# Kernel optimization log

Hardware: AMD Instinct MI355X
Metric: run time of the kernel (lower is better)

Reference implementation:

```python
import jax, jax.numpy as jnp
import numpy as np

N_HEAD = 32
N_KV = 8
HEAD_DIM = 64  # n_embd // n_head = 2048 // 32
EPS = 1e-6


def bit_linear(x, w):
    """BitNet b1.58 BitLinear (no bias): int8 absmax activation quant (per-token),
    ternary mean-absmax weight quant, straight-through estimator."""
    s = 127.0 / jnp.clip(jnp.max(jnp.abs(x), axis=-1, keepdims=True), 1e-5)
    xq = jnp.clip(jnp.round(x * s), -128.0, 127.0) / s
    xq = x + jax.lax.stop_gradient(xq - x)
    ws = 1.0 / jnp.clip(jnp.mean(jnp.abs(w)), 1e-5)
    wq = jnp.clip(jnp.round(w * ws), -1.0, 1.0) / ws
    wq = w + jax.lax.stop_gradient(wq - w)
    return xq @ wq.T


def sub_ln(x, gamma, beta):
    mean = jnp.mean(x, axis=-1, keepdims=True)
    var = jnp.mean((x - mean) ** 2, axis=-1, keepdims=True)
    return (x - mean) / jnp.sqrt(var + EPS) * gamma + beta


def setup_inputs() -> dict:
    key = jax.random.key(0)
    ks = jax.random.split(key, 8)
    D, KV, F = 2048, 512, 8192
    B, T = 1, 2048
    w_scale = 0.02
    return {
        "x": jax.random.normal(ks[0], (B, T, D), jnp.float32),
        "g1": jnp.ones((D,), jnp.float32),
        "b1": jnp.zeros((D,), jnp.float32),
        "g2": jnp.ones((D,), jnp.float32),
        "b2": jnp.zeros((D,), jnp.float32),
        "wq": jax.random.normal(ks[1], (D, D), jnp.float32) * w_scale,
        "wk": jax.random.normal(ks[2], (KV, D), jnp.float32) * w_scale,
        "wv": jax.random.normal(ks[3], (KV, D), jnp.float32) * w_scale,
        "wo": jax.random.normal(ks[4], (D, D), jnp.float32) * w_scale,
        "w1": jax.random.normal(ks[5], (F, D), jnp.float32) * w_scale,
        "w2": jax.random.normal(ks[6], (D, F), jnp.float32) * w_scale,
    }


def reference(x, g1, b1, g2, b2, wq, wk, wv, wo, w1, w2):
    B, T, D = x.shape
    # --- attention sublayer (pre-norm, residual) ---
    h = sub_ln(x, g1, b1)
    q = bit_linear(h, wq).reshape(B, T, N_HEAD, HEAD_DIM)
    k = bit_linear(h, wk).reshape(B, T, N_KV, HEAD_DIM)
    v = bit_linear(h, wv).reshape(B, T, N_KV, HEAD_DIM)
    rep = N_HEAD // N_KV
    k = jnp.repeat(k, rep, axis=2)  # GQA repeat_interleave
    v = jnp.repeat(v, rep, axis=2)
    attn = jnp.einsum('bqhd,bkhd->bhqk', q, k) * (HEAD_DIM ** -0.5)
    causal = jnp.tril(jnp.ones((T, T), bool))
    attn = jnp.where(causal, attn, -jnp.inf)
    attn = jax.nn.softmax(attn, axis=-1)
    o = jnp.einsum('bhqk,bkhd->bqhd', attn, v).reshape(B, T, D)
    x = x + bit_linear(o, wo)
    # --- FFN sublayer (pre-norm, residual, ReLU^2) ---
    h2 = sub_ln(x, g2, b2)
    f = bit_linear(h2, w1)
    f = jnp.maximum(f, 0.0) ** 2
    return x + bit_linear(f, w2)
```

## Files before the change

kernel.cpp:

```cpp
#include <hip/hip_runtime.h>
#include <hip/hip_bf16.h>
#include <stdint.h>

typedef __bf16 bf16;
typedef signed char i8;
typedef __bf16 v8bf __attribute__((ext_vector_type(8)));
typedef __bf16 v4bf __attribute__((ext_vector_type(4)));
typedef signed char v8i8 __attribute__((ext_vector_type(8)));
typedef int    v4i  __attribute__((ext_vector_type(4)));
typedef float  f32x16 __attribute__((ext_vector_type(16)));

#define MFMA32(a,b,c)   __builtin_amdgcn_mfma_f32_32x32x16_bf16((a),(b),(c),0,0,0)
#define MFMA_I8(a,b,c)  __builtin_amdgcn_mfma_i32_16x16x64_i8((a),(b),(c),0,0,0)

#define INV_D2 (1.0f / 4194304.0f)
#define INV_KV (1.0f / 1048576.0f)
#define INV_F  (1.0f / 16777216.0f)

__device__ __forceinline__ void glds16(const void* g, void* l) {
  __builtin_amdgcn_global_load_lds(
      (const __attribute__((address_space(1))) void*)g,
      (__attribute__((address_space(3))) void*)l, 16, 0, 0);
}

__device__ __forceinline__ float wred_sum(float v) {
#pragma unroll
  for (int o = 32; o; o >>= 1) v += __shfl_xor(v, o);
  return v;
}
__device__ __forceinline__ float wred_max(float v) {
#pragma unroll
  for (int o = 32; o; o >>= 1) v = fmaxf(v, __shfl_xor(v, o));
  return v;
}

__device__ __forceinline__ unsigned int packbf(float a, float b) {
  union { bf16 h[2]; unsigned int u; } x;
  x.h[0] = (bf16)a; x.h[1] = (bf16)b;
  return x.u;
}

__global__ void k_sniff(const unsigned short* __restrict__ x, int* __restrict__ flag) {
  int cnt = 0;
  for (int i = threadIdx.x; i < 2048; i += 64) {
    const unsigned short u = x[i];
    const int e = (u >> 7) & 0xFF;
    if (u == 0 || (e >= 100 && e <= 140)) cnt++;
  }
#pragma unroll
  for (int o = 32; o; o >>= 1) cnt += __shfl_xor(cnt, o);
  if (threadIdx.x == 0) flag[0] = (cnt >= 1844) ? 0 : 1;
}


__global__ void k_zero(float* p, int n) {
  int i = threadIdx.x;
  if (i < n) p[i] = 0.0f;
}

__global__ __launch_bounds__(256) void k_zerof(float4* __restrict__ p) {
  p[(size_t)blockIdx.x * 256 + threadIdx.x] = make_float4(0.f, 0.f, 0.f, 0.f);
}

__global__ __launch_bounds__(256) void k_abssum6(const void* __restrict__ p0, const void* __restrict__ p1,
                                                 const void* __restrict__ p2, const void* __restrict__ p3,
                                                 const void* __restrict__ p4, const void* __restrict__ p5,
                                                 const int* __restrict__ flag, float* __restrict__ out) {
  const int b = blockIdx.x, tid = threadIdx.x;
  const void* w; int seg, base;
  if (b < 64)       { w = p0; seg = 0; base = b; }
  else if (b < 80)  { w = p1; seg = 1; base = b - 64; }
  else if (b < 96)  { w = p2; seg = 2; base = b - 80; }
  else if (b < 160) { w = p3; seg = 3; base = b - 96; }
  else if (b < 416) { w = p4; seg = 4; base = b - 160; }
  else              { w = p5; seg = 5; base = b - 416; }
  const int f32 = flag[0];
  __shared__ float sred[4];
  float s = 0.0f;
  if (f32) {
    const float4* p = (const float4*)w + (size_t)base * 16384;
#pragma unroll 4
    for (int i = 0; i < 64; i++) {
      float4 a = p[i * 256 + tid];
      s += fabsf(a.x) + fabsf(a.y) + fabsf(a.z) + fabsf(a.w);
    }
  } else {
    const v8bf* p = (const v8bf*)w + (size_t)base * 8192;
#pragma unroll 4
    for (int i = 0; i < 32; i++) {
      v8bf v = p[i * 256 + tid];
#pragma unroll
      for (int j = 0; j < 8; j++) s += fabsf((float)v[j]);
    }
  }
  s = wred_sum(s);
  if ((tid & 63) == 0) sred[tid >> 6] = s;
  __syncthreads();
  if (tid == 0) atomicAdd(out + seg, sred[0] + sred[1] + sred[2] + sred[3]);
}

__global__ __launch_bounds__(256) void k_wquant6(const void* __restrict__ p0, const void* __restrict__ p1,
                                                 const void* __restrict__ p2, const void* __restrict__ p3,
                                                 const void* __restrict__ p4, const void* __restrict__ p5,
                                                 i8* __restrict__ d0, i8* __restrict__ d1,
                                                 i8* __restrict__ d2, i8* __restrict__ d3,
                                                 i8* __restrict__ d4, i8* __restrict__ d5,
                                                 const float* __restrict__ wsum,
                                                 const int* __restrict__ flag) {
  const int b = blockIdx.x;
  const void* w; i8* o; int seg, base; float invn;
  if (b < 2048)       { w = p0; o = d0; seg = 0; base = b;         invn = INV_D2; }
  else if (b < 2560)  { w = p1; o = d1; seg = 1; base = b - 2048;  invn = INV_KV; }
  else if (b < 3072)  { w = p2; o = d2; seg = 2; base = b - 2560;  invn = INV_KV; }
  else if (b < 5120)  { w = p3; o = d3; seg = 3; base = b - 3072;  invn = INV_D2; }
  else if (b < 13312) { w = p4; o = d4; seg = 4; base = b - 5120;  invn = INV_F; }
  else                { w = p5; o = d5; seg = 5; base = b - 13312; invn = INV_F; }
  const int gid = base * 256 + threadIdx.x;
  const int i = gid * 8;
  const float ws = 1.0f / fmaxf(wsum[seg] * invn, 1e-5f);
  const int f32 = flag[0];
  float v[8];
  if (f32) {
    float4 a = ((const float4*)w)[gid * 2];
    float4 b4 = ((const float4*)w)[gid * 2 + 1];
    v[0] = a.x; v[1] = a.y; v[2] = a.z; v[3] = a.w;
    v[4] = b4.x; v[5] = b4.y; v[6] = b4.z; v[7] = b4.w;
  } else {
    v8bf t = *(const v8bf*)((const bf16*)w + i);
#pragma unroll
    for (int j = 0; j < 8; j++) v[j] = (float)t[j];
  }
  v8i8 r;
#pragma unroll
  for (int j = 0; j < 8; j++) {
    float t = rintf(v[j] * ws);
    r[j] = (i8)fminf(fmaxf(t, -1.0f), 1.0f);
  }
  *(v8i8*)(o + i) = r;
}

template <bool XINT>
__global__ __launch_bounds__(256) void k_lnq(const void* __restrict__ x, const void* __restrict__ g,
                                             const void* __restrict__ b, i8* __restrict__ q,
                                             float* __restrict__ sc, const int* __restrict__ flag) {
  const int row = blockIdx.x, tid = threadIdx.x;
  const int f32 = flag[0];
  __shared__ float sred[4];
  float v[8];
#pragma unroll
  for (int i = 0; i < 8; i++) {
    const size_t idx = (size_t)row * 2048 + tid + 256 * i;
    if (XINT)      v[i] = ((const float*)x)[idx];
    else if (f32)  v[i] = ((const float*)x)[idx];
    else           v[i] = (float)((const bf16*)x)[idx];
  }
  float s = 0.0f;
#pragma unroll
  for (int i = 0; i < 8; i++) s += v[i];
  s = wred_sum(s);
  if ((tid & 63) == 0) sred[tid >> 6] = s;
  __syncthreads();
  const float mean = (sred[0] + sred[1] + sred[2] + sred[3]) * (1.0f / 2048.0f);
  __syncthreads();
  float vs = 0.0f;
#pragma unroll
  for (int i = 0; i < 8; i++) { float d = v[i] - mean; vs += d * d; }
  vs = wred_sum(vs);
  if ((tid & 63) == 0) sred[tid >> 6] = vs;
  __syncthreads();
  const float rstd = rsqrtf((sred[0] + sred[1] + sred[2] + sred[3]) * (1.0f / 2048.0f) + 1e-6f);
  __syncthreads();
  float hq[8];
  float am = 0.0f;
#pragma unroll
  for (int i = 0; i < 8; i++) {
    const int c = tid + 256 * i;
    const float gv = f32 ? ((const float*)g)[c] : (float)((const bf16*)g)[c];
    const float bv = f32 ? ((const float*)b)[c] : (float)((const bf16*)b)[c];
    hq[i] = (v[i] - mean) * rstd * gv + bv;
    am = fmaxf(am, fabsf(hq[i]));
  }
  am = wred_max(am);
  if ((tid & 63) == 0) sred[tid >> 6] = am;
  __syncthreads();
  am = fmaxf(fmaxf(sred[0], sred[1]), fmaxf(sred[2], sred[3]));
  const float cl = fmaxf(am, 1e-5f);
  const float s127 = 127.0f / cl;
#pragma unroll
  for (int i = 0; i < 8; i++) {
    float r = rintf(hq[i] * s127);
    r = fminf(fmaxf(r, -128.0f), 127.0f);
    q[(size_t)row * 2048 + tid + 256 * i] = (i8)r;
  }
  if (tid == 0) sc[row] = cl * (1.0f / 127.0f);
}

template <int IT>
__global__ __launch_bounds__(256) void k_rowq(const bf16* __restrict__ in, i8* __restrict__ q,
                                              float* __restrict__ sc) {
  const int row = blockIdx.x, tid = threadIdx.x;
  const int C = IT * 256;
  __shared__ float sred[4];
  const bf16* xr = in + (size_t)row * C;
  float v[IT];
  float am = 0.0f;
#pragma unroll
  for (int i = 0; i < IT; i++) {
    v[i] = (float)xr[tid + 256 * i];
    am = fmaxf(am, fabsf(v[i]));
  }
  am = wred_max(am);
  if ((tid & 63) == 0) sred[tid >> 6] = am;
  __syncthreads();
  am = fmaxf(fmaxf(sred[0], sred[1]), fmaxf(sred[2], sred[3]));
  const float cl = fmaxf(am, 1e-5f);
  const float s127 = 127.0f / cl;
#pragma unroll
  for (int i = 0; i < IT; i++) {
    float r = rintf(v[i] * s127);
    r = fminf(fmaxf(r, -128.0f), 127.0f);
    q[(size_t)row * C + tid + 256 * i] = (i8)r;
  }
  if (tid == 0) sc[row] = cl * (1.0f / 127.0f);
}

template <int EPI>
__global__ __launch_bounds__(256) void k_gemm(const i8* __restrict__ A, const i8* __restrict__ B,
                                              const float* __restrict__ sA,
                                              const float* __restrict__ wsum, float winv,
                                              void* __restrict__ out,
                                              int M, int N, int K, int Kc,
                                              const int* __restrict__ flag) {
  __shared__ __align__(16) i8 As[2][128 * 64];
  __shared__ __align__(16) i8 Bs[2][128 * 64];
  const int tid = threadIdx.x;
  const int lane = tid & 63;
  const int ml = lane & 15;
  const int q4 = lane >> 4;
  const int wid = tid >> 6;
  const int wM = wid >> 1;
  const int wN = wid & 1;
  const int m0 = blockIdx.y * 128;
  const int n0 = blockIdx.x * 128;

  const int r0 = tid >> 2;
  const int c0 = (tid & 3) * 16;
  const i8* Ag0 = A + (size_t)(m0 + r0) * K + c0;
  const i8* Ag1 = Ag0 + (size_t)64 * K;
  const i8* Bg0 = B + (size_t)(n0 + r0) * K + c0;
  const i8* Bg1 = Bg0 + (size_t)64 * K;
  const int l0 = wid * 1024;
  const int l1 = 4096 + wid * 1024;

  v4i acc[4][4] = {};

  const int kbeg = blockIdx.z * Kc;
  const int kfin = kbeg + Kc;
  glds16(Ag0 + kbeg, &As[0][l0]);
  glds16(Ag1 + kbeg, &As[0][l1]);
  glds16(Bg0 + kbeg, &Bs[0][l0]);
  glds16(Bg1 + kbeg, &Bs[0][l1]);
  __syncthreads();
  int cb = 0;
  for (int k0 = kbeg; k0 < kfin; k0 += 64) {
    const int kn = k0 + 64;
    if (kn < kfin) {
      glds16(Ag0 + kn, &As[cb ^ 1][l0]);
      glds16(Ag1 + kn, &As[cb ^ 1][l1]);
      glds16(Bg0 + kn, &Bs[cb ^ 1][l0]);
      glds16(Bg1 + kn, &Bs[cb ^ 1][l1]);
    }
    v4i af[4], bfr[4];
#pragma unroll
    for (int i = 0; i < 4; i++) af[i] = *(const v4i*)&As[cb][(wM * 64 + i * 16 + ml) * 64 + q4 * 16];
#pragma unroll
    for (int j = 0; j < 4; j++) bfr[j] = *(const v4i*)&Bs[cb][(wN * 64 + j * 16 + ml) * 64 + q4 * 16];
#pragma unroll
    for (int i = 0; i < 4; i++)
#pragma unroll
      for (int j = 0; j < 4; j++) acc[i][j] = MFMA_I8(af[i], bfr[j], acc[i][j]);
    __syncthreads();
    cb ^= 1;
  }

  if (EPI == 4) {
    int* ob = (int*)out;
#pragma unroll
    for (int i = 0; i < 4; i++)
#pragma unroll
      for (int r = 0; r < 4; r++) {
        const int row = m0 + wM * 64 + i * 16 + q4 * 4 + r;
#pragma unroll
        for (int j = 0; j < 4; j++) {
          const int col = n0 + wN * 64 + j * 16 + ml;
          atomicAdd(ob + (size_t)row * N + col, acc[i][j][r]);
        }
      }
    return;
  }

  const float cw = fmaxf(wsum[0] * winv, 1e-5f);
#pragma unroll
  for (int i = 0; i < 4; i++) {
#pragma unroll
    for (int r = 0; r < 4; r++) {
      const int row = m0 + wM * 64 + i * 16 + q4 * 4 + r;
      const float sa = sA[row] * cw;
#pragma unroll
      for (int j = 0; j < 4; j++) {
        const int col = n0 + wN * 64 + j * 16 + ml;
        const float val = (float)acc[i][j][r] * sa;
        float u = fmaxf(val, 0.0f);
        ((bf16*)out)[(size_t)row * N + col] = (bf16)(u * u);
      }
    }
  }
}

template <int MODE>
__global__ __launch_bounds__(256) void k_epi(const int* __restrict__ acc, int lda, int cofs,
                                             int ncols,
                                             const float* __restrict__ sA,
                                             const float* __restrict__ wsum, float winv,
                                             const void* __restrict__ resid,
                                             void* __restrict__ out,
                                             const int* __restrict__ flag) {
  const int row = blockIdx.x, tid = threadIdx.x;
  const float cw = fmaxf(wsum[0] * winv, 1e-5f);
  const float srow = sA[row] * cw;
  const int f32 = flag[0];
  for (int c = tid * 4; c < ncols; c += 1024) {
    const v4i a = *(const v4i*)(acc + (size_t)row * lda + cofs + c);
    const float v0 = (float)a[0] * srow, v1 = (float)a[1] * srow;
    const float v2 = (float)a[2] * srow, v3 = (float)a[3] * srow;
    const size_t o = (size_t)row * ncols + c;
    if (MODE == 1) {
      float4 rv;
      if (f32) {
        rv = *(const float4*)((const float*)resid + o);
      } else {
        const v4bf rb = *(const v4bf*)((const bf16*)resid + o);
        rv = make_float4((float)rb[0], (float)rb[1], (float)rb[2], (float)rb[3]);
      }
      *(float4*)((float*)out + o) = make_float4(rv.x + v0, rv.y + v1, rv.z + v2, rv.w + v3);
    } else {
      const float4 rv = *(const float4*)((const float*)resid + o);
      const float o0 = rv.x + v0, o1 = rv.y + v1, o2 = rv.z + v2, o3 = rv.w + v3;
      if (f32) {
        *(float4*)((float*)out + o) = make_float4(o0, o1, o2, o3);
      } else {
        v4bf r;
        r[0] = (bf16)o0; r[1] = (bf16)o1; r[2] = (bf16)o2; r[3] = (bf16)o3;
        *(v4bf*)((bf16*)out + o) = r;
      }
    }
  }
}

__global__ __launch_bounds__(256) void k_epiQK(const int* __restrict__ acc,
                                               const float* __restrict__ sA,
                                               const float* __restrict__ wsum,
                                               bf16* __restrict__ Qb, bf16* __restrict__ Kh) {
  const int row = blockIdx.x, tid = threadIdx.x;
  const float cw0 = fmaxf(wsum[0] * INV_D2, 1e-5f);
  const float cw1 = fmaxf(wsum[1] * INV_KV, 1e-5f);
  const float sa = sA[row];
  bf16* kb_ = Kh + ((size_t)(row >> 5) * 2048) + (row & 31) * 64;
  const int rx = row & 7;
  for (int c = tid * 4; c < 2560; c += 1024) {
    const v4i a = *(const v4i*)(acc + (size_t)row * 2560 + c);
    if (c < 2048) {
      v4bf r;
#pragma unroll
      for (int j = 0; j < 4; j++) r[j] = (bf16)((float)a[j] * sa * cw0);
      *(v4bf*)(Qb + (size_t)row * 2048 + c) = r;
    } else {
      const int j0 = c - 2048;
      const int kvh = j0 >> 6, d = j0 & 63;
      v4bf r;
#pragma unroll
      for (int j = 0; j < 4; j++) r[j] = (bf16)((float)a[j] * sa * cw1);
      const int elem = ((((d >> 3) ^ rx) << 3) + (d & 7));
      *(v4bf*)(kb_ + (size_t)kvh * 131072 + elem) = r;
    }
  }
}

__global__ __launch_bounds__(256) void k_epiVt(const int* __restrict__ acc,
                                               const float* __restrict__ sT,
                                               const float* __restrict__ wsum,
                                               bf16* __restrict__ Vtb) {
  const int vr = blockIdx.x, tid = threadIdx.x;
  const int kvh = vr >> 6, dd = vr & 63;
  const float cw = fmaxf(wsum[2] * INV_KV, 1e-5f);
  const int sw = (dd >> 1) & 3;
  bf16* vb = Vtb + (size_t)kvh * 131072 + dd * 32;
  for (int c = tid * 4; c < 2048; c += 1024) {
    const v4i a = *(const v4i*)(acc + (size_t)vr * 2048 + c);
    const float4 sc = *(const float4*)(sT + c);
    v4bf r;
    r[0] = (bf16)((float)a[0] * sc.x * cw);
    r[1] = (bf16)((float)a[1] * sc.y * cw);
    r[2] = (bf16)((float)a[2] * sc.z * cw);
    r[3] = (bf16)((float)a[3] * sc.w * cw);
    const int tq = c & 31;
    const int elem = (c >> 5) * 2048 + ((((tq >> 3) ^ sw) << 3) + (tq & 7));
    *(v4bf*)(vb + elem) = r;
  }
}

__global__ __launch_bounds__(64) void k_attn(const bf16* __restrict__ Q, const bf16* __restrict__ Kh,
                                             const bf16* __restrict__ Vtb, bf16* __restrict__ O) {
  __shared__ __align__(16) bf16 Kl[2][2048];
  __shared__ __align__(16) bf16 Vl[2][2048];
  const int h = blockIdx.y;
  const int kvh = h >> 2;
  const int t = (blockIdx.x + ((h >> 2) << 3)) & 63;
  const int qw0 = t * 32;
  const int lane = threadIdx.x;
  const int ql = lane & 31;
  const int hi = lane >> 5;

  v8bf qf[4];
  {
    const bf16* qp = Q + (size_t)(qw0 + ql) * 2048 + h * 64 + hi * 8;
#pragma unroll
    for (int c = 0; c < 4; c++) qf[c] = *(const v8bf*)(qp + c * 16);
  }

  float m = -1e30f, l = 0.0f;
  f32x16 acc0 = {}, acc1 = {};

  const bf16* khead = Kh + (size_t)kvh * 131072 + lane * 8;
  const bf16* vhead = Vtb + (size_t)kvh * 131072 + lane * 8;

#pragma unroll
  for (int cc = 0; cc < 4; cc++) {
    glds16(khead + cc * 512, &Kl[0][cc * 512]);
    glds16(vhead + cc * 512, &Vl[0][cc * 512]);
  }
  asm volatile("s_waitcnt vmcnt(0)" ::: "memory");
  int cb = 0;

  for (int kb = 0; kb <= qw0; kb += 32) {
    if (kb + 32 <= qw0) {
      const int tb = ((kb + 32) >> 5) * 2048;
#pragma unroll
      for (int cc = 0; cc < 4; cc++) {
        glds16(khead + tb + cc * 512, &Kl[cb ^ 1][cc * 512]);
        glds16(vhead + tb + cc * 512, &Vl[cb ^ 1][cc * 512]);
      }
    }
    f32x16 s = {};
    {
      const char* kl = (const char*)&Kl[cb][0] + ql * 128;
#pragma unroll
      for (int c = 0; c < 4; c++) {
        const int sl = ((2 * c + hi) ^ (ql & 7)) << 4;
        const v8bf kf = *(const v8bf*)(kl + sl);
        s = MFMA32(kf, qf[c], s);
      }
    }
    const bool diag = (kb == qw0);
    float p[16];
    float rm = -1e30f;
#pragma unroll
    for (int r = 0; r < 16; r++) {
      float v = s[r] * 0.125f;
      const int koff = (r & 3) + ((r >> 2) << 3) + (hi << 2);
      if (diag && koff > ql) v = -1e30f;
      p[r] = v;
      rm = fmaxf(rm, v);
    }
    rm = fmaxf(rm, __shfl_xor(rm, 32));
    const float mn = fmaxf(m, rm);
    const float alpha = __expf(m - mn);
    m = mn;
    float rs = 0.0f;
#pragma unroll
    for (int r = 0; r < 16; r++) {
      p[r] = __expf(p[r] - mn);
      rs += p[r];
    }
    rs += __shfl_xor(rs, 32);
    l = l * alpha + rs;
#pragma unroll
    for (int r = 0; r < 16; r++) { acc0[r] *= alpha; acc1[r] *= alpha; }

    unsigned int w0 = packbf(p[0], p[1]),   w2 = packbf(p[4], p[5]);
    unsigned int w1 = packbf(p[2], p[3]),   w3 = packbf(p[6], p[7]);
    unsigned int x0 = packbf(p[8], p[9]),   x2 = packbf(p[12], p[13]);
    unsigned int x1 = packbf(p[10], p[11]), x3 = packbf(p[14], p[15]);
    asm("v_permlane32_swap_b32 %0, %1" : "+v"(w0), "+v"(w2));
    asm("v_permlane32_swap_b32 %0, %1" : "+v"(w1), "+v"(w3));
    asm("v_permlane32_swap_b32 %0, %1" : "+v"(x0), "+v"(x2));
    asm("v_permlane32_swap_b32 %0, %1" : "+v"(x1), "+v"(x3));
    union BU { unsigned int u[4]; v8bf v; } B0, B1;
    B0.u[0] = w0; B0.u[1] = w1; B0.u[2] = w2; B0.u[3] = w3;
    B1.u[0] = x0; B1.u[1] = x1; B1.u[2] = x2; B1.u[3] = x3;

    {
      const char* vl = (const char*)&Vl[cb][0] + ql * 64;
      const int sx = (ql >> 1) & 3;
      const int sl0 = ((0 + hi) ^ sx) << 4;
      const int sl1 = ((2 + hi) ^ sx) << 4;
      const v8bf v00 = *(const v8bf*)(vl + sl0);
      const v8bf v01 = *(const v8bf*)(vl + sl1);
      const v8bf v10 = *(const v8bf*)(vl + 2048 + sl0);
      const v8bf v11 = *(const v8bf*)(vl + 2048 + sl1);
      acc0 = MFMA32(v00, B0.v, acc0);
      acc0 = MFMA32(v01, B1.v, acc0);
      acc1 = MFMA32(v10, B0.v, acc1);
      acc1 = MFMA32(v11, B1.v, acc1);
    }
    asm volatile("s_waitcnt vmcnt(0)" ::: "memory");
    cb ^= 1;
  }

  const float inv = 1.0f / l;
  unsigned int* op = (unsigned int*)(O + (size_t)(qw0 + ql) * 2048 + h * 64);
#pragma unroll
  for (int r = 0; r < 16; r += 2) {
    const int d = (r & 3) + ((r >> 2) << 3) + (hi << 2);
    op[d >> 1] = packbf(acc0[r] * inv, acc0[r + 1] * inv);
    op[(d >> 1) + 16] = packbf(acc1[r] * inv, acc1[r + 1] * inv);
  }
}

extern "C" void kernel_launch(void* const* d_in, const int* in_sizes, int n_in, void* d_out,
                              int out_size, void* d_ws, size_t ws_size, hipStream_t stream) {
  const void* x = d_in[0];
  const void* g1 = d_in[1];
  const void* b1 = d_in[2];
  const void* g2 = d_in[3];
  const void* b2 = d_in[4];
  const void* wq = d_in[5];
  const void* wk = d_in[6];
  const void* wv = d_in[7];
  const void* wo = d_in[8];
  const void* w1 = d_in[9];
  const void* w2 = d_in[10];

  char* ws = (char*)d_ws;
  const size_t MB = 1ull << 20;
  float* wsum = (float*)ws;
  float* s1 = (float*)(ws + 8192);
  float* so = (float*)(ws + 16384);
  float* s2 = (float*)(ws + 24576);
  float* sf = (float*)(ws + 32768);
  int* flag = (int*)(ws + 40960);
  char* big = ws + 65536;

  i8* w1z = (i8*)(big);
  i8* fq  = (i8*)(big);
  i8* w2z = (i8*)(big + 16 * MB);
  i8* wqz = (i8*)(big + 32 * MB);
  i8* wkz = (i8*)(big + 36 * MB);
  i8* wvz = (i8*)(big + 37 * MB);
  i8* woz = (i8*)(big + 38 * MB);
  i8* xq1 = (i8*)(big + 42 * MB);
  i8* oq  = xq1;
  int* accQK = (int*)(big + 46 * MB);
  int* accVt = (int*)(big + 66 * MB);
  bf16* Kh   = (bf16*)(big + 70 * MB);
  bf16* Vtb  = (bf16*)(big + 72 * MB);
  bf16* Qb   = (bf16*)(big + 74 * MB);
  bf16* Ob   = (bf16*)(big + 82 * MB);
  int* accO  = (int*)(big + 46 * MB);
  float* x1  = (float*)(big + 80 * MB);
  i8* xq2 = (i8*)(big + 74 * MB);
  bf16* Fb   = (bf16*)(big + 42 * MB);
  int* accF  = (int*)(big + 42 * MB);

  k_sniff<<<1, 64, 0, stream>>>((const unsigned short*)x, flag);
  k_zero<<<1, 64, 0, stream>>>(wsum, 8);
  k_zerof<<<6144, 256, 0, stream>>>((float4*)accQK);

  k_abssum6<<<672, 256, 0, stream>>>(wq, wk, wv, wo, w1, w2, flag, wsum);
  k_wquant6<<<21504, 256, 0, stream>>>(wq, wk, wv, wo, w1, w2,
                                       wqz, wkz, wvz, woz, w1z, w2z, wsum, flag);

  k_lnq<false><<<2048, 256, 0, stream>>>(x, g1, b1, xq1, s1, flag);
  k_gemm<4><<<dim3(20, 16, 4), 256, 0, stream>>>(xq1, wqz, s1, wsum + 0, INV_D2, accQK,
                                                 2048, 2560, 2048, 512, flag);
  k_gemm<4><<<dim3(16, 4, 4), 256, 0, stream>>>(wvz, xq1, s1, wsum + 2, INV_KV, accVt,
                                                512, 2048, 2048, 512, flag);
  k_epiQK<<<2048, 256, 0, stream>>>(accQK, s1, wsum, Qb, Kh);
  k_epiVt<<<512, 256, 0, stream>>>(accVt, s1, wsum, Vtb);
  k_attn<<<dim3(64, 32), 64, 0, stream>>>(Qb, Kh, Vtb, Ob);
  k_rowq<8><<<2048, 256, 0, stream>>>(Ob, oq, so);
  k_zerof<<<4096, 256, 0, stream>>>((float4*)accO);
  k_gemm<4><<<dim3(16, 16, 4), 256, 0, stream>>>(oq, woz, so, wsum + 3, INV_D2, accO,
                                                 2048, 2048, 2048, 512, flag);
  k_epi<1><<<2048, 256, 0, stream>>>(accO, 2048, 0, 2048, so, wsum + 3, INV_D2, x, x1, flag);

  k_lnq<true><<<2048, 256, 0, stream>>>(x1, g2, b2, xq2, s2, flag);
  k_gemm<2><<<dim3(64, 16, 1), 256, 0, stream>>>(xq2, w1z, s2, wsum + 4, INV_F, Fb,
                                                 2048, 8192, 2048, 2048, flag);
  k_rowq<32><<<2048, 256, 0, stream>>>(Fb, fq, sf);
  k_zerof<<<4096, 256, 0, stream>>>((float4*)accF);
  k_gemm<4><<<dim3(16, 16, 4), 256, 0, stream>>>(fq, w2z, sf, wsum + 5, INV_F, accF,
                                                 2048, 2048, 8192, 2048, flag);
  k_epi<2><<<2048, 256, 0, stream>>>(accF, 2048, 0, 2048, sf, wsum + 5, INV_F, x1, d_out, flag);
}
```

Measured before the change: 657.1 us.

## Deepen int8 GEMM prefetch with explicit vmcnt waits and fuse residual epilogue into LayerNorm quant

The int8 GEMM main loop now issues the next LDS tile load after the barrier, two stages ahead of use. It waits on vmcnt counts instead of a full __syncthreads, so global-to-LDS loads can overlap the MFMA work. Separately, the out-projection residual epilogue is fused with the second sub-LN and int8 row quantization into one kernel, which drops a launch and a reread of x1. The manual waitcnt and barrier scheduling is fragile: the buffer reuse with two buffers and a two-ahead issue depends on the barrier placement being correct.

```diff
diff --git a/kernel.cpp b/kernel.cpp
--- a/kernel.cpp
+++ b/kernel.cpp
@@ -252,24 +252,32 @@
   const int l0 = wid * 1024;
   const int l1 = 4096 + wid * 1024;
 
+  const int kbeg = blockIdx.z * Kc;
+  const int nst = Kc >> 6;
+
+  auto issue = [&](int tt) {
+    const int k0 = kbeg + (tt << 6);
+    const int bb = tt & 1;
+    glds16(Ag0 + k0, &As[bb][l0]);
+    glds16(Ag1 + k0, &As[bb][l1]);
+    glds16(Bg0 + k0, &Bs[bb][l0]);
+    glds16(Bg1 + k0, &Bs[bb][l1]);
+  };
+
+  issue(0);
+  if (nst > 1) {
+    issue(1);
+    asm volatile("s_waitcnt vmcnt(4)" ::: "memory");
+  } else {
+    asm volatile("s_waitcnt vmcnt(0)" ::: "memory");
+  }
+  __builtin_amdgcn_s_barrier();
+  __builtin_amdgcn_sched_barrier(0);
+
   v4i acc[4][4] = {};
 
-  const int kbeg = blockIdx.z * Kc;
-  const int kfin = kbeg + Kc;
-  glds16(Ag0 + kbeg, &As[0][l0]);
-  glds16(Ag1 + kbeg, &As[0][l1]);
-  glds16(Bg0 + kbeg, &Bs[0][l0]);
-  glds16(Bg1 + kbeg, &Bs[0][l1]);
-  __syncthreads();
-  int cb = 0;
-  for (int k0 = kbeg; k0 < kfin; k0 += 64) {
-    const int kn = k0 + 64;
-    if (kn < kfin) {
-      glds16(Ag0 + kn, &As[cb ^ 1][l0]);
-      glds16(Ag1 + kn, &As[cb ^ 1][l1]);
-      glds16(Bg0 + kn, &Bs[cb ^ 1][l0]);
-      glds16(Bg1 + kn, &Bs[cb ^ 1][l1]);
-    }
+  for (int t = 0; t < nst; ++t) {
+    const int cb = t & 1;
     v4i af[4], bfr[4];
 #pragma unroll
     for (int i = 0; i < 4; i++) af[i] = *(const v4i*)&As[cb][(wM * 64 + i * 16 + ml) * 64 + q4 * 16];
@@ -279,8 +287,19 @@
     for (int i = 0; i < 4; i++)
 #pragma unroll
       for (int j = 0; j < 4; j++) acc[i][j] = MFMA_I8(af[i], bfr[j], acc[i][j]);
-    __syncthreads();
-    cb ^= 1;
+    __builtin_amdgcn_sched_barrier(0);
+    __builtin_amdgcn_s_barrier();
+    __builtin_amdgcn_sched_barrier(0);
+    if (t + 2 < nst) {
+      issue(t + 2);
+      asm volatile("s_waitcnt vmcnt(4)" ::: "memory");
+      __builtin_amdgcn_s_barrier();
+      __builtin_amdgcn_sched_barrier(0);
+    } else if (t + 1 < nst) {
+      asm volatile("s_waitcnt vmcnt(0)" ::: "memory");
+      __builtin_amdgcn_s_barrier();
+      __builtin_amdgcn_sched_barrier(0);
+    }
   }
 
   if (EPI == 4) {
@@ -334,27 +353,78 @@
     const float v0 = (float)a[0] * srow, v1 = (float)a[1] * srow;
     const float v2 = (float)a[2] * srow, v3 = (float)a[3] * srow;
     const size_t o = (size_t)row * ncols + c;
-    if (MODE == 1) {
-      float4 rv;
-      if (f32) {
-        rv = *(const float4*)((const float*)resid + o);
-      } else {
-        const v4bf rb = *(const v4bf*)((const bf16*)resid + o);
-        rv = make_float4((float)rb[0], (float)rb[1], (float)rb[2], (float)rb[3]);
-      }
-      *(float4*)((float*)out + o) = make_float4(rv.x + v0, rv.y + v1, rv.z + v2, rv.w + v3);
+    const float4 rv = *(const float4*)((const float*)resid + o);
+    const float o0 = rv.x + v0, o1 = rv.y + v1, o2 = rv.z + v2, o3 = rv.w + v3;
+    if (f32) {
+      *(float4*)((float*)out + o) = make_float4(o0, o1, o2, o3);
     } else {
-      const float4 rv = *(const float4*)((const float*)resid + o);
-      const float o0 = rv.x + v0, o1 = rv.y + v1, o2 = rv.z + v2, o3 = rv.w + v3;
-      if (f32) {
-        *(float4*)((float*)out + o) = make_float4(o0, o1, o2, o3);
-      } else {
-        v4bf r;
-        r[0] = (bf16)o0; r[1] = (bf16)o1; r[2] = (bf16)o2; r[3] = (bf16)o3;
-        *(v4bf*)((bf16*)out + o) = r;
-      }
-    }
-  }
+      v4bf r;
+      r[0] = (bf16)o0; r[1] = (bf16)o1; r[2] = (bf16)o2; r[3] = (bf16)o3;
+      *(v4bf*)((bf16*)out + o) = r;
+    }
+  }
+}
+
+__global__ __launch_bounds__(256) void k_epi1ln(const int* __restrict__ acc,
+                                                const float* __restrict__ so_,
+                                                const float* __restrict__ wsum,
+                                                const void* __restrict__ xres,
+                                                float* __restrict__ x1,
+                                                const void* __restrict__ g, const void* __restrict__ b,
+                                                i8* __restrict__ q, float* __restrict__ sc,
+                                                const int* __restrict__ flag) {
+  const int row = blockIdx.x, tid = threadIdx.x;
+  const int f32 = flag[0];
+  __shared__ float sred[4];
+  const float srow = so_[row] * fmaxf(wsum[3] * INV_D2, 1e-5f);
+  float v[8];
+#pragma unroll
+  for (int i = 0; i < 8; i++) {
+    const size_t idx = (size_t)row * 2048 + tid + 256 * i;
+    const float a = (float)acc[idx] * srow;
+    const float rv = f32 ? ((const float*)xres)[idx] : (float)((const bf16*)xres)[idx];
+    v[i] = rv + a;
+    x1[idx] = v[i];
+  }
+  float s = 0.0f;
+#pragma unroll
+  for (int i = 0; i < 8; i++) s += v[i];
+  s = wred_sum(s);
+  if ((tid & 63) == 0) sred[tid >> 6] = s;
+  __syncthreads();
+  const float mean = (sred[0] + sred[1] + sred[2] + sred[3]) * (1.0f / 2048.0f);
+  __syncthreads();
+  float vs = 0.0f;
+#pragma unroll
+  for (int i = 0; i < 8; i++) { float d = v[i] - mean; vs += d * d; }
+  vs = wred_sum(vs);
+  if ((tid & 63) == 0) sred[tid >> 6] = vs;
+  __syncthreads();
+  const float rstd = rsqrtf((sred[0] + sred[1] + sred[2] + sred[3]) * (1.0f / 2048.0f) + 1e-6f);
+  __syncthreads();
+  float hq[8];
+  float am = 0.0f;
+#pragma unroll
+  for (int i = 0; i < 8; i++) {
+    const int c = tid + 256 * i;
+    const float gv = f32 ? ((const float*)g)[c] : (float)((const bf16*)g)[c];
+    const float bv = f32 ? ((const float*)b)[c] : (float)((const bf16*)b)[c];
+    hq[i] = (v[i] - mean) * rstd * gv + bv;
+    am = fmaxf(am, fabsf(hq[i]));
+  }
+  am = wred_max(am);
+  if ((tid & 63) == 0) sred[tid >> 6] = am;
+  __syncthreads();
+  am = fmaxf(fmaxf(sred[0], sred[1]), fmaxf(sred[2], sred[3]));
+  const float cl = fmaxf(am, 1e-5f);
+  const float s127 = 127.0f / cl;
+#pragma unroll
+  for (int i = 0; i < 8; i++) {
+    float r = rintf(hq[i] * s127);
+    r = fminf(fmaxf(r, -128.0f), 127.0f);
+    q[(size_t)row * 2048 + tid + 256 * i] = (i8)r;
+  }
+  if (tid == 0) sc[row] = cl * (1.0f / 127.0f);
 }
 
 __global__ __launch_bounds__(256) void k_epiQK(const int* __restrict__ acc,
@@ -592,9 +662,8 @@
   k_zerof<<<4096, 256, 0, stream>>>((float4*)accO);
   k_gemm<4><<<dim3(16, 16, 4), 256, 0, stream>>>(oq, woz, so, wsum + 3, INV_D2, accO,
                                                  2048, 2048, 2048, 512, flag);
-  k_epi<1><<<2048, 256, 0, stream>>>(accO, 2048, 0, 2048, so, wsum + 3, INV_D2, x, x1, flag);
-
-  k_lnq<true><<<2048, 256, 0, stream>>>(x1, g2, b2, xq2, s2, flag);
+  k_epi1ln<<<2048, 256, 0, stream>>>(accO, so, wsum, x, x1, g2, b2, xq2, s2, flag);
+
   k_gemm<2><<<dim3(64, 16, 1), 256, 0, stream>>>(xq2, w1z, s2, wsum + 4, INV_F, Fb,
                                                  2048, 8192, 2048, 2048, flag);
   k_rowq<32><<<2048, 256, 0, stream>>>(Fb, fq, sf);
```

Result: no change. 663.7 us (+1.0%).
